# Optimization experiments

Hardware: AMD Instinct MI355X
Metric: run time of the kernel (lower is better)

## Reference

```python
import jax, jax.numpy as jnp
import numpy as np

T, B, I, H = 512, 64, 256, 512

def setup_inputs() -> dict:
    key = jax.random.key(0)
    ks = jax.random.split(key, 5)
    s = 0.1  # matches uniform(-0.1, 0.1) init scale
    return {
        "x": jax.random.normal(ks[0], (T, B, I), dtype=jnp.float32),
        "weight_ih": jax.random.uniform(ks[1], (H, I), dtype=jnp.float32, minval=-s, maxval=s),
        "weight_hh": jax.random.uniform(ks[2], (H, H), dtype=jnp.float32, minval=-s, maxval=s),
        "bias_ih": jax.random.uniform(ks[3], (H,), dtype=jnp.float32, minval=-s, maxval=s),
        "bias_hh": jax.random.uniform(ks[4], (H,), dtype=jnp.float32, minval=-s, maxval=s),
    }

def reference(x, weight_ih, weight_hh, bias_ih, bias_hh):
    # Precompute input contribution for all timesteps in one big GEMM: [T,B,H]
    xw = jnp.einsum('tbi,hi->tbh', x, weight_ih) + bias_ih + bias_hh
    h0 = jnp.zeros((x.shape[1], weight_hh.shape[0]), dtype=x.dtype)

    def step(h, xw_t):
        h = jax.nn.relu(xw_t + h @ weight_hh.T)
        return h, h

    h_final, output = jax.lax.scan(step, h0, xw)
    return output, h_final
```

## Files before the change

### kernel.cpp

```cpp
#include <hip/hip_runtime.h>

#define T_DIM 512
#define B_DIM 64
#define I_DIM 256
#define H_DIM 512
#define BH_DIM (B_DIM * H_DIM)


__global__ __launch_bounds__(256) void xw_gemm(
    const float* __restrict__ x, const float* __restrict__ wih,
    const float* __restrict__ bih, const float* __restrict__ bhh,
    float* __restrict__ out) {
  __shared__ __align__(16) float As[32][128];
  __shared__ __align__(16) float Bs[32][128];

  const int bm = blockIdx.x >> 2;
  const int bn = blockIdx.x & 3;
  const int m0 = bm * 128, n0 = bn * 128;
  const int tid = threadIdx.x;
  const int tx = tid & 15, ty = tid >> 4;
  const int ml = tid & 127, kq = tid >> 7;

  float acc[8][8];
#pragma unroll
  for (int r = 0; r < 8; r++)
#pragma unroll
    for (int c = 0; c < 8; c++) acc[r][c] = 0.f;

  for (int kc = 0; kc < I_DIM; kc += 32) {
    const float4* xr = (const float4*)(x + (size_t)(m0 + ml) * I_DIM + kc + kq * 16);
    const float4* br = (const float4*)(wih + (size_t)(n0 + ml) * I_DIM + kc + kq * 16);
    float4 av[4], bv[4];
#pragma unroll
    for (int j = 0; j < 4; j++) { av[j] = xr[j]; bv[j] = br[j]; }

    __syncthreads();
#pragma unroll
    for (int j = 0; j < 4; j++) {
      const int k = kq * 16 + j * 4;
      As[k + 0][ml] = av[j].x; As[k + 1][ml] = av[j].y;
      As[k + 2][ml] = av[j].z; As[k + 3][ml] = av[j].w;
      Bs[k + 0][ml] = bv[j].x; Bs[k + 1][ml] = bv[j].y;
      Bs[k + 2][ml] = bv[j].z; Bs[k + 3][ml] = bv[j].w;
    }
    __syncthreads();

#pragma unroll 4
    for (int kk = 0; kk < 32; kk++) {
      const float4 a0 = *(const float4*)&As[kk][ty * 4];
      const float4 a1 = *(const float4*)&As[kk][64 + ty * 4];
      const float4 b0 = *(const float4*)&Bs[kk][tx * 4];
      const float4 b1 = *(const float4*)&Bs[kk][64 + tx * 4];
      const float ar[8] = {a0.x, a0.y, a0.z, a0.w, a1.x, a1.y, a1.z, a1.w};
      const float br_[8] = {b0.x, b0.y, b0.z, b0.w, b1.x, b1.y, b1.z, b1.w};
#pragma unroll
      for (int r = 0; r < 8; r++)
#pragma unroll
        for (int c = 0; c < 8; c++) acc[r][c] = fmaf(ar[r], br_[c], acc[r][c]);
    }
  }

  const float4 bi0 = *(const float4*)(bih + n0 + tx * 4);
  const float4 bh0 = *(const float4*)(bhh + n0 + tx * 4);
  const float4 bi1 = *(const float4*)(bih + n0 + 64 + tx * 4);
  const float4 bh1 = *(const float4*)(bhh + n0 + 64 + tx * 4);
  const float4 bb0 = make_float4(bi0.x + bh0.x, bi0.y + bh0.y, bi0.z + bh0.z, bi0.w + bh0.w);
  const float4 bb1 = make_float4(bi1.x + bh1.x, bi1.y + bh1.y, bi1.z + bh1.z, bi1.w + bh1.w);

#pragma unroll
  for (int r = 0; r < 8; r++) {
    const int m = m0 + ((r < 4) ? (ty * 4 + r) : (64 + ty * 4 + (r - 4)));
    float4* orow = (float4*)(out + (size_t)m * H_DIM + n0);
    orow[tx] = make_float4(acc[r][0] + bb0.x, acc[r][1] + bb0.y,
                           acc[r][2] + bb0.z, acc[r][3] + bb0.w);
    orow[16 + tx] = make_float4(acc[r][4] + bb1.x, acc[r][5] + bb1.y,
                                acc[r][6] + bb1.z, acc[r][7] + bb1.w);
  }
}


__device__ __forceinline__ float row16_sum(float v) {
  int m;
  m = __builtin_amdgcn_update_dpp(0, __float_as_int(v), 0xB1, 0xF, 0xF, true);
  v += __int_as_float(m);
  m = __builtin_amdgcn_update_dpp(0, __float_as_int(v), 0x4E, 0xF, 0xF, true);
  v += __int_as_float(m);
  m = __builtin_amdgcn_update_dpp(0, __float_as_int(v), 0x124, 0xF, 0xF, true);
  v += __int_as_float(m);
  m = __builtin_amdgcn_update_dpp(0, __float_as_int(v), 0x128, 0xF, 0xF, true);
  v += __int_as_float(m);
  return v;
}

__global__ __launch_bounds__(512, 2) void rnn_scan(
    const float* __restrict__ whh, float* __restrict__ out,
    unsigned long long* __restrict__ stage) {
  __shared__ __align__(16) float hbuf[2][H_DIM];

  const int b   = blockIdx.x & 63;
  const int rb  = blockIdx.x >> 6;
  const int tid = threadIdx.x;
  const int rg  = tid >> 4;
  const int cg  = tid & 15;
  const int j0  = rb * 128 + rg * 4;

  const int pj = (tid < rb * 128) ? tid : tid + 128;

  float4 w[4][8];
#pragma unroll
  for (int r = 0; r < 4; r++) {
    const float4* wr = (const float4*)(whh + (size_t)(j0 + r) * H_DIM);
#pragma unroll
    for (int i = 0; i < 8; i++) w[r][i] = wr[i * 16 + cg];
  }

  float* __restrict__ outb = out + (size_t)b * H_DIM;
  unsigned long long* __restrict__ stg0 = stage + (size_t)b * H_DIM;
  unsigned long long* __restrict__ stg1 = stage + (size_t)(64 + b) * H_DIM;

  float hlast = 0.f;

  if (cg < 4) {
    const int j = j0 + cg;
    const float h = fmaxf(__builtin_nontemporal_load(&outb[j]), 0.f);
    union { float f; unsigned int u; } cv; cv.f = h;
    __hip_atomic_store(&stg0[j], (1ULL << 32) | (unsigned long long)cv.u,
                       __ATOMIC_RELAXED, __HIP_MEMORY_SCOPE_AGENT);
    __builtin_nontemporal_store(h, &outb[j]);
    hbuf[0][j] = h;
    hlast = h;
  }

  for (int t = 1; t < T_DIM; t++) {
    const int p = (t - 1) & 1;
    float* hb = hbuf[p];
    float* o_t = outb + (size_t)t * BH_DIM;

    if (tid < 384) {
      unsigned long long* slot = (p ? stg1 : stg0) + pj;
      const unsigned int want = (unsigned int)t;
      unsigned long long v;
      do {
        v = __hip_atomic_load(slot, __ATOMIC_RELAXED, __HIP_MEMORY_SCOPE_AGENT);
      } while ((unsigned int)(v >> 32) != want);
      union { unsigned int u; float f; } cv; cv.u = (unsigned int)v;
      hb[pj] = cv.f;
    }

    float xwv = 0.f;
    if (cg < 4) xwv = __builtin_nontemporal_load(&o_t[j0 + cg]);

    __syncthreads();

    float a0 = 0.f, a1 = 0.f, a2 = 0.f, a3 = 0.f;
#pragma unroll
    for (int i = 0; i < 8; i++) {
      const float4 hv = ((const float4*)hb)[i * 16 + cg];
      a0 = fmaf(w[0][i].x, hv.x, a0); a0 = fmaf(w[0][i].y, hv.y, a0);
      a0 = fmaf(w[0][i].z, hv.z, a0); a0 = fmaf(w[0][i].w, hv.w, a0);
      a1 = fmaf(w[1][i].x, hv.x, a1); a1 = fmaf(w[1][i].y, hv.y, a1);
      a1 = fmaf(w[1][i].z, hv.z, a1); a1 = fmaf(w[1][i].w, hv.w, a1);
      a2 = fmaf(w[2][i].x, hv.x, a2); a2 = fmaf(w[2][i].y, hv.y, a2);
      a2 = fmaf(w[2][i].z, hv.z, a2); a2 = fmaf(w[2][i].w, hv.w, a2);
      a3 = fmaf(w[3][i].x, hv.x, a3); a3 = fmaf(w[3][i].y, hv.y, a3);
      a3 = fmaf(w[3][i].z, hv.z, a3); a3 = fmaf(w[3][i].w, hv.w, a3);
    }

    a0 = row16_sum(a0);
    a1 = row16_sum(a1);
    a2 = row16_sum(a2);
    a3 = row16_sum(a3);

    if (cg < 4) {
      const float acc = (cg == 0) ? a0 : (cg == 1) ? a1 : (cg == 2) ? a2 : a3;
      const float h = fmaxf(acc + xwv, 0.f);
      const int j = j0 + cg;
      union { float f; unsigned int u; } cv; cv.f = h;
      const unsigned long long val =
          ((unsigned long long)(unsigned int)(t + 1) << 32) |
          (unsigned long long)cv.u;
      unsigned long long* sb = (t & 1) ? stg1 : stg0;
      __hip_atomic_store(&sb[j], val, __ATOMIC_RELAXED,
                         __HIP_MEMORY_SCOPE_AGENT);
      __builtin_nontemporal_store(h, &o_t[j]);
      hbuf[t & 1][j] = h;
      hlast = h;
    }
  }

  if (cg < 4) {
    __builtin_nontemporal_store(
        hlast, &out[(size_t)T_DIM * BH_DIM + (size_t)b * H_DIM + j0 + cg]);
  }
}

extern "C" void kernel_launch(void* const* d_in, const int* in_sizes, int n_in,
                              void* d_out, int out_size, void* d_ws, size_t ws_size,
                              hipStream_t stream) {
  const float* x   = (const float*)d_in[0];
  const float* wih = (const float*)d_in[1];
  const float* whh = (const float*)d_in[2];
  const float* bih = (const float*)d_in[3];
  const float* bhh = (const float*)d_in[4];
  float* out = (float*)d_out;
  unsigned long long* stage = (unsigned long long*)d_ws;

  xw_gemm<<<1024, 256, 0, stream>>>(x, wih, bih, bhh, out);
  rnn_scan<<<256, 512, 0, stream>>>(whh, out, stage);
}
```

Baseline: 887.8 us.

## Interleave two batch rows per scan block to overlap cross-block waits with compute

The scan kernel now gives each block two batch rows instead of one and alternates between them. While one row's hidden state is being computed, the block is already waiting on the other row's staged values from peer blocks. It also issues each row's first poll speculatively and prefetches the next step's input projection. This halves the grid to 128 blocks and is meant to hide inter-block synchronisation latency on the serial recurrence, at the cost of doubling per-block work and adding a second barrier per step.

```diff
diff --git a/kernel.cpp b/kernel.cpp
--- a/kernel.cpp
+++ b/kernel.cpp
@@ -92,17 +92,42 @@
   return v;
 }
 
-__global__ __launch_bounds__(512, 2) void rnn_scan(
+__device__ __forceinline__ float hh_acc(const float* hb,
+                                        const float4 (&w)[4][8], int cg) {
+  float a0 = 0.f, a1 = 0.f, a2 = 0.f, a3 = 0.f;
+#pragma unroll
+  for (int i = 0; i < 8; i++) {
+    const float4 hv = ((const float4*)hb)[i * 16 + cg];
+    a0 = fmaf(w[0][i].x, hv.x, a0); a0 = fmaf(w[0][i].y, hv.y, a0);
+    a0 = fmaf(w[0][i].z, hv.z, a0); a0 = fmaf(w[0][i].w, hv.w, a0);
+    a1 = fmaf(w[1][i].x, hv.x, a1); a1 = fmaf(w[1][i].y, hv.y, a1);
+    a1 = fmaf(w[1][i].z, hv.z, a1); a1 = fmaf(w[1][i].w, hv.w, a1);
+    a2 = fmaf(w[2][i].x, hv.x, a2); a2 = fmaf(w[2][i].y, hv.y, a2);
+    a2 = fmaf(w[2][i].z, hv.z, a2); a2 = fmaf(w[2][i].w, hv.w, a2);
+    a3 = fmaf(w[3][i].x, hv.x, a3); a3 = fmaf(w[3][i].y, hv.y, a3);
+    a3 = fmaf(w[3][i].z, hv.z, a3); a3 = fmaf(w[3][i].w, hv.w, a3);
+  }
+  a0 = row16_sum(a0);
+  a1 = row16_sum(a1);
+  a2 = row16_sum(a2);
+  a3 = row16_sum(a3);
+  return (cg == 0) ? a0 : (cg == 1) ? a1 : (cg == 2) ? a2 : a3;
+}
+
+__global__ __launch_bounds__(512, 2) void rnn_scan2(
     const float* __restrict__ whh, float* __restrict__ out,
     unsigned long long* __restrict__ stage) {
-  __shared__ __align__(16) float hbuf[2][H_DIM];
-
-  const int b   = blockIdx.x & 63;
-  const int rb  = blockIdx.x >> 6;
+  __shared__ __align__(16) float hbA[2][H_DIM];
+  __shared__ __align__(16) float hbB[2][H_DIM];
+
+  const int k   = blockIdx.x & 31;
+  const int rb  = blockIdx.x >> 5;
+  const int b0  = 2 * k, b1 = 2 * k + 1;
   const int tid = threadIdx.x;
   const int rg  = tid >> 4;
   const int cg  = tid & 15;
   const int j0  = rb * 128 + rg * 4;
+  const int jj  = j0 + cg;
 
   const int pj = (tid < rb * 128) ? tid : tid + 128;
 
@@ -114,83 +139,122 @@
     for (int i = 0; i < 8; i++) w[r][i] = wr[i * 16 + cg];
   }
 
-  float* __restrict__ outb = out + (size_t)b * H_DIM;
-  unsigned long long* __restrict__ stg0 = stage + (size_t)b * H_DIM;
-  unsigned long long* __restrict__ stg1 = stage + (size_t)(64 + b) * H_DIM;
-
-  float hlast = 0.f;
+  float* __restrict__ outA = out + (size_t)b0 * H_DIM;
+  float* __restrict__ outB = out + (size_t)b1 * H_DIM;
+  unsigned long long* __restrict__ stgA0 = stage + (size_t)b0 * H_DIM;
+  unsigned long long* __restrict__ stgA1 = stage + (size_t)(64 + b0) * H_DIM;
+  unsigned long long* __restrict__ stgB0 = stage + (size_t)b1 * H_DIM;
+  unsigned long long* __restrict__ stgB1 = stage + (size_t)(64 + b1) * H_DIM;
+
+  float hlastA = 0.f, hlastB = 0.f;
 
   if (cg < 4) {
-    const int j = j0 + cg;
-    const float h = fmaxf(__builtin_nontemporal_load(&outb[j]), 0.f);
-    union { float f; unsigned int u; } cv; cv.f = h;
-    __hip_atomic_store(&stg0[j], (1ULL << 32) | (unsigned long long)cv.u,
+    const float hA = fmaxf(outA[jj], 0.f);
+    const float hB = fmaxf(outB[jj], 0.f);
+    union { float f; unsigned int u; } ca, cb; ca.f = hA; cb.f = hB;
+    __hip_atomic_store(&stgA0[jj], (1ULL << 32) | (unsigned long long)ca.u,
                        __ATOMIC_RELAXED, __HIP_MEMORY_SCOPE_AGENT);
-    __builtin_nontemporal_store(h, &outb[j]);
-    hbuf[0][j] = h;
-    hlast = h;
-  }
+    __hip_atomic_store(&stgB0[jj], (1ULL << 32) | (unsigned long long)cb.u,
+                       __ATOMIC_RELAXED, __HIP_MEMORY_SCOPE_AGENT);
+    __builtin_nontemporal_store(hA, &outA[jj]);
+    __builtin_nontemporal_store(hB, &outB[jj]);
+    hbA[0][jj] = hA;
+    hbB[0][jj] = hB;
+    hlastA = hA;
+    hlastB = hB;
+  }
+
+  float xwA_cur = 0.f, xwB_cur = 0.f;
+  if (cg < 4) {
+    xwA_cur = __builtin_nontemporal_load(&outA[(size_t)BH_DIM + jj]);
+    xwB_cur = __builtin_nontemporal_load(&outB[(size_t)BH_DIM + jj]);
+  }
+
+  unsigned long long vA = 0;
+  if (tid < 384)
+    vA = __hip_atomic_load(stgA0 + pj, __ATOMIC_RELAXED,
+                           __HIP_MEMORY_SCOPE_AGENT);
 
   for (int t = 1; t < T_DIM; t++) {
     const int p = (t - 1) & 1;
-    float* hb = hbuf[p];
-    float* o_t = outb + (size_t)t * BH_DIM;
+    const unsigned int want = (unsigned int)t;
+    float* o_tA = outA + (size_t)t * BH_DIM;
+    float* o_tB = outB + (size_t)t * BH_DIM;
 
     if (tid < 384) {
-      unsigned long long* slot = (p ? stg1 : stg0) + pj;
-      const unsigned int want = (unsigned int)t;
-      unsigned long long v;
-      do {
-        v = __hip_atomic_load(slot, __ATOMIC_RELAXED, __HIP_MEMORY_SCOPE_AGENT);
-      } while ((unsigned int)(v >> 32) != want);
+      unsigned long long* slot = (p ? stgA1 : stgA0) + pj;
+      unsigned long long v = vA;
+      while ((unsigned int)(v >> 32) != want)
+        v = __hip_atomic_load(slot, __ATOMIC_RELAXED,
+                              __HIP_MEMORY_SCOPE_AGENT);
       union { unsigned int u; float f; } cv; cv.u = (unsigned int)v;
-      hb[pj] = cv.f;
-    }
-
-    float xwv = 0.f;
-    if (cg < 4) xwv = __builtin_nontemporal_load(&o_t[j0 + cg]);
-
-    __syncthreads();
-
-    float a0 = 0.f, a1 = 0.f, a2 = 0.f, a3 = 0.f;
-#pragma unroll
-    for (int i = 0; i < 8; i++) {
-      const float4 hv = ((const float4*)hb)[i * 16 + cg];
-      a0 = fmaf(w[0][i].x, hv.x, a0); a0 = fmaf(w[0][i].y, hv.y, a0);
-      a0 = fmaf(w[0][i].z, hv.z, a0); a0 = fmaf(w[0][i].w, hv.w, a0);
-      a1 = fmaf(w[1][i].x, hv.x, a1); a1 = fmaf(w[1][i].y, hv.y, a1);
-      a1 = fmaf(w[1][i].z, hv.z, a1); a1 = fmaf(w[1][i].w, hv.w, a1);
-      a2 = fmaf(w[2][i].x, hv.x, a2); a2 = fmaf(w[2][i].y, hv.y, a2);
-      a2 = fmaf(w[2][i].z, hv.z, a2); a2 = fmaf(w[2][i].w, hv.w, a2);
-      a3 = fmaf(w[3][i].x, hv.x, a3); a3 = fmaf(w[3][i].y, hv.y, a3);
-      a3 = fmaf(w[3][i].z, hv.z, a3); a3 = fmaf(w[3][i].w, hv.w, a3);
-    }
-
-    a0 = row16_sum(a0);
-    a1 = row16_sum(a1);
-    a2 = row16_sum(a2);
-    a3 = row16_sum(a3);
-
+      hbA[p][pj] = cv.f;
+    }
+    __syncthreads();
+
+    unsigned long long vB = 0;
+    if (tid < 384)
+      vB = __hip_atomic_load((p ? stgB1 : stgB0) + pj, __ATOMIC_RELAXED,
+                             __HIP_MEMORY_SCOPE_AGENT);
+
+    const float accA = hh_acc(hbA[p], w, cg);
     if (cg < 4) {
-      const float acc = (cg == 0) ? a0 : (cg == 1) ? a1 : (cg == 2) ? a2 : a3;
-      const float h = fmaxf(acc + xwv, 0.f);
-      const int j = j0 + cg;
+      const float h = fmaxf(accA + xwA_cur, 0.f);
       union { float f; unsigned int u; } cv; cv.f = h;
-      const unsigned long long val =
-          ((unsigned long long)(unsigned int)(t + 1) << 32) |
-          (unsigned long long)cv.u;
-      unsigned long long* sb = (t & 1) ? stg1 : stg0;
-      __hip_atomic_store(&sb[j], val, __ATOMIC_RELAXED,
-                         __HIP_MEMORY_SCOPE_AGENT);
-      __builtin_nontemporal_store(h, &o_t[j]);
-      hbuf[t & 1][j] = h;
-      hlast = h;
-    }
+      unsigned long long* sb = (t & 1) ? stgA1 : stgA0;
+      __hip_atomic_store(&sb[jj],
+                         ((unsigned long long)(unsigned int)(t + 1) << 32) |
+                             (unsigned long long)cv.u,
+                         __ATOMIC_RELAXED, __HIP_MEMORY_SCOPE_AGENT);
+      __builtin_nontemporal_store(h, &o_tA[jj]);
+      hbA[t & 1][jj] = h;
+      hlastA = h;
+    }
+
+    if (tid < 384) {
+      unsigned long long* slot = (p ? stgB1 : stgB0) + pj;
+      unsigned long long v = vB;
+      while ((unsigned int)(v >> 32) != want)
+        v = __hip_atomic_load(slot, __ATOMIC_RELAXED,
+                              __HIP_MEMORY_SCOPE_AGENT);
+      union { unsigned int u; float f; } cv; cv.u = (unsigned int)v;
+      hbB[p][pj] = cv.f;
+    }
+    __syncthreads();
+
+    float xwA_n = 0.f, xwB_n = 0.f;
+    if (cg < 4 && t + 1 < T_DIM) {
+      xwA_n = __builtin_nontemporal_load(&outA[(size_t)(t + 1) * BH_DIM + jj]);
+      xwB_n = __builtin_nontemporal_load(&outB[(size_t)(t + 1) * BH_DIM + jj]);
+    }
+
+    const float accB = hh_acc(hbB[p], w, cg);
+    if (cg < 4) {
+      const float h = fmaxf(accB + xwB_cur, 0.f);
+      union { float f; unsigned int u; } cv; cv.f = h;
+      unsigned long long* sb = (t & 1) ? stgB1 : stgB0;
+      __hip_atomic_store(&sb[jj],
+                         ((unsigned long long)(unsigned int)(t + 1) << 32) |
+                             (unsigned long long)cv.u,
+                         __ATOMIC_RELAXED, __HIP_MEMORY_SCOPE_AGENT);
+      __builtin_nontemporal_store(h, &o_tB[jj]);
+      hbB[t & 1][jj] = h;
+      hlastB = h;
+    }
+
+    if (tid < 384)
+      vA = __hip_atomic_load(((t & 1) ? stgA1 : stgA0) + pj, __ATOMIC_RELAXED,
+                             __HIP_MEMORY_SCOPE_AGENT);
+
+    xwA_cur = xwA_n;
+    xwB_cur = xwB_n;
   }
 
   if (cg < 4) {
     __builtin_nontemporal_store(
-        hlast, &out[(size_t)T_DIM * BH_DIM + (size_t)b * H_DIM + j0 + cg]);
+        hlastA, &out[(size_t)T_DIM * BH_DIM + (size_t)b0 * H_DIM + jj]);
+    __builtin_nontemporal_store(
+        hlastB, &out[(size_t)T_DIM * BH_DIM + (size_t)b1 * H_DIM + jj]);
   }
 }
 
@@ -206,5 +270,5 @@
   unsigned long long* stage = (unsigned long long*)d_ws;
 
   xw_gemm<<<1024, 256, 0, stream>>>(x, wih, bih, bhh, out);
-  rnn_scan<<<256, 512, 0, stream>>>(whh, out, stage);
-}
+  rnn_scan2<<<128, 512, 0, stream>>>(whh, out, stage);
+}
```

Measured after the change: 963.2 us. 1.08x slower.

## Poll two stage slots per thread, prefetch next xw and issue early stage loads

Applied to the files above, without the earlier changes.

The recurrent scan kernel now has 192 poller threads, each reading two adjacent staged h values instead of 384 threads reading one each. It issues the first poll loads for the next step right after publishing the current h, so the load latency overlaps the rest of the iteration. The xw input for step t+1 is loaded one step ahead to take it off the critical path. In exchange, fewer threads carry the polling traffic and a speculative load can return stale data, which then forces another spin round.

```diff
diff --git a/kernel.cpp b/kernel.cpp
--- a/kernel.cpp
+++ b/kernel.cpp
@@ -92,7 +92,29 @@
   return v;
 }
 
-__global__ __launch_bounds__(512, 2) void rnn_scan(
+__device__ __forceinline__ float hh_acc(const float* hb,
+                                        const float4 (&w)[4][8], int cg) {
+  float a0 = 0.f, a1 = 0.f, a2 = 0.f, a3 = 0.f;
+#pragma unroll
+  for (int i = 0; i < 8; i++) {
+    const float4 hv = ((const float4*)hb)[i * 16 + cg];
+    a0 = fmaf(w[0][i].x, hv.x, a0); a0 = fmaf(w[0][i].y, hv.y, a0);
+    a0 = fmaf(w[0][i].z, hv.z, a0); a0 = fmaf(w[0][i].w, hv.w, a0);
+    a1 = fmaf(w[1][i].x, hv.x, a1); a1 = fmaf(w[1][i].y, hv.y, a1);
+    a1 = fmaf(w[1][i].z, hv.z, a1); a1 = fmaf(w[1][i].w, hv.w, a1);
+    a2 = fmaf(w[2][i].x, hv.x, a2); a2 = fmaf(w[2][i].y, hv.y, a2);
+    a2 = fmaf(w[2][i].z, hv.z, a2); a2 = fmaf(w[2][i].w, hv.w, a2);
+    a3 = fmaf(w[3][i].x, hv.x, a3); a3 = fmaf(w[3][i].y, hv.y, a3);
+    a3 = fmaf(w[3][i].z, hv.z, a3); a3 = fmaf(w[3][i].w, hv.w, a3);
+  }
+  a0 = row16_sum(a0);
+  a1 = row16_sum(a1);
+  a2 = row16_sum(a2);
+  a3 = row16_sum(a3);
+  return (cg == 0) ? a0 : (cg == 1) ? a1 : (cg == 2) ? a2 : a3;
+}
+
+__global__ __launch_bounds__(512, 2) void rnn_scan3(
     const float* __restrict__ whh, float* __restrict__ out,
     unsigned long long* __restrict__ stage) {
   __shared__ __align__(16) float hbuf[2][H_DIM];
@@ -103,8 +125,10 @@
   const int rg  = tid >> 4;
   const int cg  = tid & 15;
   const int j0  = rb * 128 + rg * 4;
-
-  const int pj = (tid < rb * 128) ? tid : tid + 128;
+  const int jj  = j0 + cg;
+
+  const int pjp = (tid < rb * 64) ? tid : tid + 64;
+  const bool poller = (tid < 192);
 
   float4 w[4][8];
 #pragma unroll
@@ -121,76 +145,80 @@
   float hlast = 0.f;
 
   if (cg < 4) {
-    const int j = j0 + cg;
-    const float h = fmaxf(__builtin_nontemporal_load(&outb[j]), 0.f);
+    const float h = fmaxf(outb[jj], 0.f);
     union { float f; unsigned int u; } cv; cv.f = h;
-    __hip_atomic_store(&stg0[j], (1ULL << 32) | (unsigned long long)cv.u,
+    __hip_atomic_store(&stg0[jj], (1ULL << 32) | (unsigned long long)cv.u,
                        __ATOMIC_RELAXED, __HIP_MEMORY_SCOPE_AGENT);
-    __builtin_nontemporal_store(h, &outb[j]);
-    hbuf[0][j] = h;
+    __builtin_nontemporal_store(h, &outb[jj]);
+    hbuf[0][jj] = h;
     hlast = h;
   }
+
+  unsigned long long* slot = stg0 + 2 * pjp;
+  unsigned long long v0 = 0, v1 = 0;
+  if (poller) {
+    v0 = __hip_atomic_load(slot, __ATOMIC_RELAXED, __HIP_MEMORY_SCOPE_AGENT);
+    v1 = __hip_atomic_load(slot + 1, __ATOMIC_RELAXED,
+                           __HIP_MEMORY_SCOPE_AGENT);
+  }
+  float xwv = 0.f;
+  if (cg < 4)
+    xwv = __builtin_nontemporal_load(&outb[(size_t)BH_DIM + jj]);
 
   for (int t = 1; t < T_DIM; t++) {
     const int p = (t - 1) & 1;
-    float* hb = hbuf[p];
+    const unsigned int want = (unsigned int)t;
     float* o_t = outb + (size_t)t * BH_DIM;
 
-    if (tid < 384) {
-      unsigned long long* slot = (p ? stg1 : stg0) + pj;
-      const unsigned int want = (unsigned int)t;
-      unsigned long long v;
-      do {
-        v = __hip_atomic_load(slot, __ATOMIC_RELAXED, __HIP_MEMORY_SCOPE_AGENT);
-      } while ((unsigned int)(v >> 32) != want);
-      union { unsigned int u; float f; } cv; cv.u = (unsigned int)v;
-      hb[pj] = cv.f;
-    }
-
-    float xwv = 0.f;
-    if (cg < 4) xwv = __builtin_nontemporal_load(&o_t[j0 + cg]);
+    if (poller) {
+      while ((unsigned int)(v0 >> 32) != want ||
+             (unsigned int)(v1 >> 32) != want) {
+        v0 = __hip_atomic_load(slot, __ATOMIC_RELAXED,
+                               __HIP_MEMORY_SCOPE_AGENT);
+        v1 = __hip_atomic_load(slot + 1, __ATOMIC_RELAXED,
+                               __HIP_MEMORY_SCOPE_AGENT);
+      }
+      union { unsigned int u; float f; } c0, c1;
+      c0.u = (unsigned int)v0; c1.u = (unsigned int)v1;
+      hbuf[p][2 * pjp] = c0.f;
+      hbuf[p][2 * pjp + 1] = c1.f;
+    }
 
     __syncthreads();
 
-    float a0 = 0.f, a1 = 0.f, a2 = 0.f, a3 = 0.f;
-#pragma unroll
-    for (int i = 0; i < 8; i++) {
-      const float4 hv = ((const float4*)hb)[i * 16 + cg];
-      a0 = fmaf(w[0][i].x, hv.x, a0); a0 = fmaf(w[0][i].y, hv.y, a0);
-      a0 = fmaf(w[0][i].z, hv.z, a0); a0 = fmaf(w[0][i].w, hv.w, a0);
-      a1 = fmaf(w[1][i].x, hv.x, a1); a1 = fmaf(w[1][i].y, hv.y, a1);
-      a1 = fmaf(w[1][i].z, hv.z, a1); a1 = fmaf(w[1][i].w, hv.w, a1);
-      a2 = fmaf(w[2][i].x, hv.x, a2); a2 = fmaf(w[2][i].y, hv.y, a2);
-      a2 = fmaf(w[2][i].z, hv.z, a2); a2 = fmaf(w[2][i].w, hv.w, a2);
-      a3 = fmaf(w[3][i].x, hv.x, a3); a3 = fmaf(w[3][i].y, hv.y, a3);
-      a3 = fmaf(w[3][i].z, hv.z, a3); a3 = fmaf(w[3][i].w, hv.w, a3);
-    }
-
-    a0 = row16_sum(a0);
-    a1 = row16_sum(a1);
-    a2 = row16_sum(a2);
-    a3 = row16_sum(a3);
+    float xw_n = 0.f;
+    if (cg < 4 && t + 1 < T_DIM)
+      xw_n = __builtin_nontemporal_load(&outb[(size_t)(t + 1) * BH_DIM + jj]);
+
+    const float acc = hh_acc(hbuf[p], w, cg);
 
     if (cg < 4) {
-      const float acc = (cg == 0) ? a0 : (cg == 1) ? a1 : (cg == 2) ? a2 : a3;
       const float h = fmaxf(acc + xwv, 0.f);
-      const int j = j0 + cg;
       union { float f; unsigned int u; } cv; cv.f = h;
-      const unsigned long long val =
-          ((unsigned long long)(unsigned int)(t + 1) << 32) |
-          (unsigned long long)cv.u;
       unsigned long long* sb = (t & 1) ? stg1 : stg0;
-      __hip_atomic_store(&sb[j], val, __ATOMIC_RELAXED,
-                         __HIP_MEMORY_SCOPE_AGENT);
-      __builtin_nontemporal_store(h, &o_t[j]);
-      hbuf[t & 1][j] = h;
+      __hip_atomic_store(&sb[jj],
+                         ((unsigned long long)(unsigned int)(t + 1) << 32) |
+                             (unsigned long long)cv.u,
+                         __ATOMIC_RELAXED, __HIP_MEMORY_SCOPE_AGENT);
+      __builtin_nontemporal_store(h, &o_t[jj]);
+      hbuf[t & 1][jj] = h;
       hlast = h;
     }
+
+    if (poller) {
+      slot = ((t & 1) ? stg1 : stg0) + 2 * pjp;
+      v0 = __hip_atomic_load(slot, __ATOMIC_RELAXED,
+                             __HIP_MEMORY_SCOPE_AGENT);
+      v1 = __hip_atomic_load(slot + 1, __ATOMIC_RELAXED,
+                             __HIP_MEMORY_SCOPE_AGENT);
+    }
+
+    xwv = xw_n;
   }
 
   if (cg < 4) {
     __builtin_nontemporal_store(
-        hlast, &out[(size_t)T_DIM * BH_DIM + (size_t)b * H_DIM + j0 + cg]);
+        hlast, &out[(size_t)T_DIM * BH_DIM + (size_t)b * H_DIM + jj]);
   }
 }
 
@@ -206,5 +234,5 @@
   unsigned long long* stage = (unsigned long long*)d_ws;
 
   xw_gemm<<<1024, 256, 0, stream>>>(x, wih, bih, bhh, out);
-  rnn_scan<<<256, 512, 0, stream>>>(whh, out, stage);
-}
+  rnn_scan3<<<256, 512, 0, stream>>>(whh, out, stage);
+}
```

Measured after the change: 1.003 ms. +13.0%, slower.
